# Kernel optimization log

Hardware: AMD Instinct MI355X
Metric: run time of the kernel (lower is better)

Reference implementation:

```python
import jax, jax.numpy as jnp
import numpy as np

NUM_LEVELS = 8
CODEBOOK_SIZE = 1024
D_MODEL = 512


def setup_inputs() -> dict:
    key = jax.random.key(0)
    kx, kc = jax.random.split(key)
    x = jax.random.normal(kx, (8, 4096, D_MODEL), dtype=jnp.float32)
    # stacked embedding tables, one per RVQ level: [L, K, D]
    codebooks = jax.random.normal(kc, (NUM_LEVELS, CODEBOOK_SIZE, D_MODEL), dtype=jnp.float32)
    return {"x": x, "codebooks": codebooks}


def reference(x, codebooks):
    """Residual VQ: per level, nearest-codebook lookup on the residual.

    x: [B, N, D], codebooks: [L, K, D].
    Returns (quantized [B, N, D] with straight-through estimator, indices [B, N, L]).
    """
    residual = x
    q_sum = jnp.zeros_like(x)
    all_indices = []
    for l in range(codebooks.shape[0]):
        cb = codebooks[l]  # [K, D]
        # squared Euclidean distance; argmin matches torch.cdist argmin
        r2 = jnp.sum(residual * residual, axis=-1, keepdims=True)      # [B, N, 1]
        c2 = jnp.sum(cb * cb, axis=-1)                                  # [K]
        cross = jnp.einsum("bnd,kd->bnk", residual, cb)                # [B, N, K]
        dist2 = r2 - 2.0 * cross + c2                                   # [B, N, K]
        idx = jnp.argmin(dist2, axis=-1)                                # [B, N]
        all_indices.append(idx)
        q = cb[idx]                                                     # gather: [B, N, D]
        q_sum = q_sum + q
        residual = residual - q
    # straight-through: forward value is q_sum, gradient flows to x only
    quantized = x + jax.lax.stop_gradient(q_sum - x)
    return quantized, jnp.stack(all_indices, axis=-1)
```

## Files before the change

kernel.cpp:

```cpp
#include <hip/hip_runtime.h>
#include <stdint.h>

#define NLV 8
#define KCB 1024
#define DM  512
#define NTOK (8*4096)
#define BETA 0.00390625f

typedef _Float16 f16;
typedef f16  f16x4 __attribute__((ext_vector_type(4)));
typedef f16  f16x8 __attribute__((ext_vector_type(8)));
typedef float f32x4 __attribute__((ext_vector_type(4)));

typedef __attribute__((address_space(1))) const unsigned int* as1p;
typedef __attribute__((address_space(3))) unsigned int*       as3p;
__device__ __forceinline__ void gll16(const void* g, void* l) {
    __builtin_amdgcn_global_load_lds((as1p)g, (as3p)l, 16, 0, 0);
}

#define VMCNT(n) asm volatile("s_waitcnt vmcnt(" #n ")" ::: "memory")

__global__ void c2_kernel(const float* __restrict__ cbs, float* __restrict__ c2) {
    int row  = blockIdx.x;
    int lane = threadIdx.x;
    const float4* p4 = (const float4*)(cbs + (size_t)row * DM);
    float4 a = p4[lane];
    float4 b = p4[lane + 64];
    float s = a.x*a.x + a.y*a.y + a.z*a.z + a.w*a.w
            + b.x*b.x + b.y*b.y + b.z*b.z + b.w*b.w;
    float t = (float)(f16)a.x + (float)(f16)a.y + (float)(f16)a.z + (float)(f16)a.w
            + (float)(f16)b.x + (float)(f16)b.y + (float)(f16)b.z + (float)(f16)b.w;
    #pragma unroll
    for (int off = 32; off > 0; off >>= 1) {
        s += __shfl_down(s, off, 64);
        t += __shfl_down(t, off, 64);
    }
    if (lane == 0) c2[row] = s + 2.0f * BETA * t;
}

__global__ void split_kernel(const float* __restrict__ src,
                             f16* __restrict__ hi, f16* __restrict__ lo) {
    size_t i = (size_t)blockIdx.x * 256 + threadIdx.x;
    float4 v = ((const float4*)src)[i];
    f16x4 h, l;
    h.x = (f16)v.x; l.x = (f16)((v.x - (float)h.x) + BETA);
    h.y = (f16)v.y; l.y = (f16)((v.y - (float)h.y) + BETA);
    h.z = (f16)v.z; l.z = (f16)((v.z - (float)h.z) + BETA);
    h.w = (f16)v.w; l.w = (f16)((v.w - (float)h.w) + BETA);
    ((f16x4*)hi)[i] = h;
    ((f16x4*)lo)[i] = l;
}

#define MBT  64
#define NCH  256
#define KS   32
#define NTHR 256
#define BUFB 40960

__global__ __launch_bounds__(NTHR, 2)
void rvq_mfma(const float* __restrict__ xin, float* __restrict__ qout,
              const float* __restrict__ cbs,
              const f16* __restrict__ Bhi, const f16* __restrict__ Blo,
              f16* __restrict__ Ahi, f16* __restrict__ Alo,
              const float* __restrict__ c2g, float* __restrict__ idxout,
              int lvl, int is_last)
{
    __shared__ char smem[2 * BUFB];
    const int tid  = threadIdx.x;
    const int lane = tid & 63;
    const int wn   = tid >> 6;
    const int tx   = lane & 15;
    const int q    = lane >> 4;
    const size_t tok0 = (size_t)blockIdx.x * MBT;

    const f16*   Bh_l = Bhi + (size_t)lvl * KCB * DM;
    const f16*   Bl_l = Blo + (size_t)lvl * KCB * DM;
    const float* c2l  = c2g + lvl * KCB;
    const float* cbl  = cbs + (size_t)lvl * KCB * DM;

    const int srow = tid >> 2;
    const int sg   = (tid & 3) ^ ((srow >> 1) & 3);
    const int rsw  = q ^ ((tx >> 1) & 3);

    auto stageA = [&](char* buf, int gk2) {
        const int ko = (gk2 & 15) * KS + sg * 8;
        char* wb = buf + wn * 1024;
        const size_t ga = (tok0 + srow) * (size_t)DM + ko;
        gll16(&Ahi[ga], wb);
        gll16(&Alo[ga], wb + 4096);
    };
    auto stageBh = [&](char* buf, int gk2) {
        const int cb0 = (gk2 >> 4) * NCH;
        const int ko  = (gk2 & 15) * KS + sg * 8;
        char* wb = buf + wn * 1024;
        #pragma unroll
        for (int i = 0; i < 4; ++i)
            gll16(&Bh_l[(size_t)(cb0 + 64 * i + srow) * DM + ko], wb + 8192 + 4096 * i);
    };
    auto stageBl = [&](char* buf, int gk2) {
        const int cb0 = (gk2 >> 4) * NCH;
        const int ko  = (gk2 & 15) * KS + sg * 8;
        char* wb = buf + wn * 1024;
        #pragma unroll
        for (int i = 0; i < 4; ++i)
            gll16(&Bl_l[(size_t)(cb0 + 64 * i + srow) * DM + ko], wb + 24576 + 4096 * i);
    };

    int aoff[4], boff[4];
    #pragma unroll
    for (int i = 0; i < 4; ++i) aoff[i] = (i * 16 + tx) * 64 + rsw * 16;
    #pragma unroll
    for (int j = 0; j < 4; ++j) boff[j] = (wn * 64 + j * 16 + tx) * 64 + rsw * 16;

    float bestv[16];
    int   besti[16];
    #pragma unroll
    for (int t = 0; t < 16; ++t) { bestv[t] = 3.4e38f; besti[t] = 0; }

    stageA(smem, 0); stageBh(smem, 0); stageBl(smem, 0);

    for (int ch = 0; ch < KCB / NCH; ++ch) {
        f32x4 acc[4][4];
        #pragma unroll
        for (int i = 0; i < 4; ++i)
            #pragma unroll
            for (int j = 0; j < 4; ++j) acc[i][j] = (f32x4)0.0f;

        for (int kk = 0; kk < 16; ++kk) {
            const int gk = ch * 16 + kk;
            const int nx = (gk + 1) & 63;
            char* bb = smem + (gk & 1) * BUFB;
            char* bn = smem + ((gk & 1) ^ 1) * BUFB;

            stageA(bn, nx);
            __builtin_amdgcn_sched_barrier(0);
            VMCNT(2);
            __builtin_amdgcn_s_barrier();
            __builtin_amdgcn_sched_barrier(0);

            f16x8 ah[4], al[4], bh[4], bl[4];
            #pragma unroll
            for (int i = 0; i < 4; ++i) ah[i] = *(const f16x8*)(bb + aoff[i]);
            #pragma unroll
            for (int j = 0; j < 4; ++j) bh[j] = *(const f16x8*)(bb + 8192 + boff[j]);

            __builtin_amdgcn_s_setprio(1);
            #pragma unroll
            for (int j = 0; j < 4; ++j)
                #pragma unroll
                for (int i = 0; i < 4; ++i)
                    acc[i][j] = __builtin_amdgcn_mfma_f32_16x16x32_f16(ah[i], bh[j], acc[i][j], 0, 0, 0);
            __builtin_amdgcn_s_setprio(0);

            stageBh(bn, nx);
            __builtin_amdgcn_s_barrier();

            #pragma unroll
            for (int j = 0; j < 4; ++j) bl[j] = *(const f16x8*)(bb + 24576 + boff[j]);

            __builtin_amdgcn_s_setprio(1);
            #pragma unroll
            for (int j = 0; j < 4; ++j)
                #pragma unroll
                for (int i = 0; i < 4; ++i)
                    acc[i][j] = __builtin_amdgcn_mfma_f32_16x16x32_f16(ah[i], bl[j], acc[i][j], 0, 0, 0);
            __builtin_amdgcn_s_setprio(0);

            stageBl(bn, nx);
            __builtin_amdgcn_s_barrier();

            #pragma unroll
            for (int i = 0; i < 4; ++i) al[i] = *(const f16x8*)(bb + 4096 + aoff[i]);

            __builtin_amdgcn_s_setprio(1);
            #pragma unroll
            for (int j = 0; j < 4; ++j)
                #pragma unroll
                for (int i = 0; i < 4; ++i)
                    acc[i][j] = __builtin_amdgcn_mfma_f32_16x16x32_f16(al[i], bh[j], acc[i][j], 0, 0, 0);
            __builtin_amdgcn_s_setprio(0);
        }

        const int cb0 = ch * NCH;
        #pragma unroll
        for (int j = 0; j < 4; ++j) {
            int n = cb0 + wn * 64 + j * 16 + tx;
            float c2v = c2l[n];
            #pragma unroll
            for (int i = 0; i < 4; ++i)
                #pragma unroll
                for (int r = 0; r < 4; ++r) {
                    float s = fmaf(-2.f, acc[i][j][r], c2v);
                    int t = i * 4 + r;
                    if (s < bestv[t]) { bestv[t] = s; besti[t] = n; }
                }
        }
    }

    #pragma unroll
    for (int t = 0; t < 16; ++t) {
        float v = bestv[t]; int bi = besti[t];
        #pragma unroll
        for (int off = 1; off < 16; off <<= 1) {
            float ov = __shfl_xor(v, off, 64);
            int   oi = __shfl_xor(bi, off, 64);
            if (ov < v || (ov == v && oi < bi)) { v = ov; bi = oi; }
        }
        bestv[t] = v; besti[t] = bi;
    }

    float* redV = (float*)smem;
    int*   redI = (int*)(smem + 1024);
    int*   kbst = (int*)(smem + 2048);
    __syncthreads();
    if (tx == 0) {
        #pragma unroll
        for (int i = 0; i < 4; ++i)
            #pragma unroll
            for (int r = 0; r < 4; ++r) {
                int m = i * 16 + q * 4 + r;
                redV[wn * 64 + m] = bestv[i * 4 + r];
                redI[wn * 64 + m] = besti[i * 4 + r];
            }
    }
    __syncthreads();
    if (tid < MBT) {
        float bv = redV[tid]; int bi = redI[tid];
        #pragma unroll
        for (int w = 1; w < 4; ++w) {
            float v  = redV[w * 64 + tid];
            int   ii = redI[w * 64 + tid];
            if (v < bv || (v == bv && ii < bi)) { bv = v; bi = ii; }
        }
        kbst[tid] = bi;
        idxout[(tok0 + tid) * NLV + lvl] = (float)bi;
    }
    __syncthreads();

    #pragma unroll 4
    for (int it = 0; it < 16; ++it) {
        int e  = it * NTHR + tid;
        int t  = e >> 6, d8 = e & 63;
        size_t go = (tok0 + t) * (size_t)DM + d8 * 8;
        f16x8 h8 = *(const f16x8*)&Ahi[go];
        f16x8 l8 = *(const f16x8*)&Alo[go];
        const float* cp = &cbl[(size_t)kbst[t] * DM + d8 * 8];
        float4 c0 = *(const float4*)cp;
        float4 c1 = *(const float4*)(cp + 4);
        float r[8];
        r[0] = (float)h8[0] + ((float)l8[0] - BETA) - c0.x;
        r[1] = (float)h8[1] + ((float)l8[1] - BETA) - c0.y;
        r[2] = (float)h8[2] + ((float)l8[2] - BETA) - c0.z;
        r[3] = (float)h8[3] + ((float)l8[3] - BETA) - c0.w;
        r[4] = (float)h8[4] + ((float)l8[4] - BETA) - c1.x;
        r[5] = (float)h8[5] + ((float)l8[5] - BETA) - c1.y;
        r[6] = (float)h8[6] + ((float)l8[6] - BETA) - c1.z;
        r[7] = (float)h8[7] + ((float)l8[7] - BETA) - c1.w;
        if (is_last) {
            float4 x0 = *(const float4*)&xin[go];
            float4 x1 = *(const float4*)&xin[go + 4];
            float4 q0 = make_float4(x0.x - r[0], x0.y - r[1], x0.z - r[2], x0.w - r[3]);
            float4 q1 = make_float4(x1.x - r[4], x1.y - r[5], x1.z - r[6], x1.w - r[7]);
            *(float4*)&qout[go]     = q0;
            *(float4*)&qout[go + 4] = q1;
        } else {
            f16x8 h, l;
            #pragma unroll
            for (int k = 0; k < 8; ++k) {
                h[k] = (f16)r[k];
                l[k] = (f16)((r[k] - (float)h[k]) + BETA);
            }
            *(f16x8*)&Ahi[go] = h;
            *(f16x8*)&Alo[go] = l;
        }
    }
}

extern "C" void kernel_launch(void* const* d_in, const int* in_sizes, int n_in,
                              void* d_out, int out_size, void* d_ws, size_t ws_size,
                              hipStream_t stream) {
    const float* x   = (const float*)d_in[0];
    const float* cbs = (const float*)d_in[1];
    float* qout   = (float*)d_out;
    float* idxout = qout + (size_t)NTOK * DM;

    const size_t B_ELE = (size_t)NLV * KCB * DM;
    const size_t A_ELE = (size_t)NTOK * DM;

    f16* Bhi = (f16*)d_ws;
    f16* Blo = Bhi + B_ELE;
    f16* Ahi = Blo + B_ELE;
    f16* Alo = Ahi + A_ELE;
    float* c2 = (float*)(Alo + A_ELE);

    split_kernel<<<(int)(B_ELE / 4 / 256), 256, 0, stream>>>(cbs, Bhi, Blo);
    split_kernel<<<(int)(A_ELE / 4 / 256), 256, 0, stream>>>(x, Ahi, Alo);
    c2_kernel<<<NLV * KCB, 64, 0, stream>>>(cbs, c2);

    const int nblocks = NTOK / MBT;
    for (int l = 0; l < NLV; ++l) {
        rvq_mfma<<<nblocks, NTHR, 0, stream>>>(x, qout, cbs,
                                               Bhi, Blo, Ahi, Alo, c2, idxout,
                                               l, (l == NLV - 1) ? 1 : 0);
    }
}
```

Before: 1.147 ms.

## Load codebook B fragments directly into registers, keep only A in LDS

```diff
diff --git a/kernel.cpp b/kernel.cpp
--- a/kernel.cpp
+++ b/kernel.cpp
@@ -55,7 +55,7 @@
 #define NCH  256
 #define KS   32
 #define NTHR 256
-#define BUFB 40960
+#define ABUF 8192
 
 __global__ __launch_bounds__(NTHR, 2)
 void rvq_mfma(const float* __restrict__ xin, float* __restrict__ qout,
@@ -65,7 +65,7 @@
               const float* __restrict__ c2g, float* __restrict__ idxout,
               int lvl, int is_last)
 {
-    __shared__ char smem[2 * BUFB];
+    __shared__ char smem[2 * ABUF];
     const int tid  = threadIdx.x;
     const int lane = tid & 63;
     const int wn   = tid >> 6;
@@ -82,42 +82,45 @@
     const int sg   = (tid & 3) ^ ((srow >> 1) & 3);
     const int rsw  = q ^ ((tx >> 1) & 3);
 
+    const f16* pA0 = Ahi + (tok0 + srow) * (size_t)DM + sg * 8;
+    const f16* pL0 = Alo + (tok0 + srow) * (size_t)DM + sg * 8;
+
     auto stageA = [&](char* buf, int gk2) {
-        const int ko = (gk2 & 15) * KS + sg * 8;
+        const int kOff = (gk2 & 15) * KS;
         char* wb = buf + wn * 1024;
-        const size_t ga = (tok0 + srow) * (size_t)DM + ko;
-        gll16(&Ahi[ga], wb);
-        gll16(&Alo[ga], wb + 4096);
+        gll16(pA0 + kOff, wb);
+        gll16(pL0 + kOff, wb + 4096);
     };
-    auto stageBh = [&](char* buf, int gk2) {
-        const int cb0 = (gk2 >> 4) * NCH;
-        const int ko  = (gk2 & 15) * KS + sg * 8;
-        char* wb = buf + wn * 1024;
-        #pragma unroll
-        for (int i = 0; i < 4; ++i)
-            gll16(&Bh_l[(size_t)(cb0 + 64 * i + srow) * DM + ko], wb + 8192 + 4096 * i);
+
+    int loffB[4];
+    #pragma unroll
+    for (int j = 0; j < 4; ++j)
+        loffB[j] = (wn * 64 + j * 16 + tx) * DM + q * 8;
+
+    auto loadB = [&](int gk2, f16x8 (&bh)[4], f16x8 (&bl)[4]) {
+        const int sOff = ((gk2 >> 4) * NCH) * DM + (gk2 & 15) * KS;
+        const f16* pbh = Bh_l + sOff;
+        const f16* pbl = Bl_l + sOff;
+        #pragma unroll
+        for (int j = 0; j < 4; ++j) {
+            bh[j] = *(const f16x8*)(pbh + loffB[j]);
+            bl[j] = *(const f16x8*)(pbl + loffB[j]);
+        }
     };
-    auto stageBl = [&](char* buf, int gk2) {
-        const int cb0 = (gk2 >> 4) * NCH;
-        const int ko  = (gk2 & 15) * KS + sg * 8;
-        char* wb = buf + wn * 1024;
-        #pragma unroll
-        for (int i = 0; i < 4; ++i)
-            gll16(&Bl_l[(size_t)(cb0 + 64 * i + srow) * DM + ko], wb + 24576 + 4096 * i);
-    };
-
-    int aoff[4], boff[4];
+
+    int aoff[4];
     #pragma unroll
     for (int i = 0; i < 4; ++i) aoff[i] = (i * 16 + tx) * 64 + rsw * 16;
-    #pragma unroll
-    for (int j = 0; j < 4; ++j) boff[j] = (wn * 64 + j * 16 + tx) * 64 + rsw * 16;
 
     float bestv[16];
     int   besti[16];
     #pragma unroll
     for (int t = 0; t < 16; ++t) { bestv[t] = 3.4e38f; besti[t] = 0; }
 
-    stageA(smem, 0); stageBh(smem, 0); stageBl(smem, 0);
+    f16x8 bhE[4], blE[4], bhO[4], blO[4];
+
+    loadB(0, bhE, blE);
+    stageA(smem, 0);
 
     for (int ch = 0; ch < KCB / NCH; ++ch) {
         f32x4 acc[4][4];
@@ -126,59 +129,48 @@
             #pragma unroll
             for (int j = 0; j < 4; ++j) acc[i][j] = (f32x4)0.0f;
 
-        for (int kk = 0; kk < 16; ++kk) {
-            const int gk = ch * 16 + kk;
+        auto kbody = [&](int gk, f16x8 (&bhc)[4], f16x8 (&blc)[4],
+                         f16x8 (&bhn)[4], f16x8 (&bln)[4]) {
             const int nx = (gk + 1) & 63;
-            char* bb = smem + (gk & 1) * BUFB;
-            char* bn = smem + ((gk & 1) ^ 1) * BUFB;
-
+            char* bb = smem + (gk & 1) * ABUF;
+            char* bn = smem + ((gk & 1) ^ 1) * ABUF;
+
+            loadB(nx, bhn, bln);
             stageA(bn, nx);
             __builtin_amdgcn_sched_barrier(0);
-            VMCNT(2);
+            VMCNT(10);
             __builtin_amdgcn_s_barrier();
             __builtin_amdgcn_sched_barrier(0);
 
-            f16x8 ah[4], al[4], bh[4], bl[4];
+            f16x8 ah[4], al[4];
             #pragma unroll
             for (int i = 0; i < 4; ++i) ah[i] = *(const f16x8*)(bb + aoff[i]);
             #pragma unroll
-            for (int j = 0; j < 4; ++j) bh[j] = *(const f16x8*)(bb + 8192 + boff[j]);
+            for (int i = 0; i < 4; ++i) al[i] = *(const f16x8*)(bb + 4096 + aoff[i]);
 
             __builtin_amdgcn_s_setprio(1);
             #pragma unroll
             for (int j = 0; j < 4; ++j)
                 #pragma unroll
                 for (int i = 0; i < 4; ++i)
-                    acc[i][j] = __builtin_amdgcn_mfma_f32_16x16x32_f16(ah[i], bh[j], acc[i][j], 0, 0, 0);
+                    acc[i][j] = __builtin_amdgcn_mfma_f32_16x16x32_f16(ah[i], bhc[j], acc[i][j], 0, 0, 0);
+            #pragma unroll
+            for (int j = 0; j < 4; ++j)
+                #pragma unroll
+                for (int i = 0; i < 4; ++i)
+                    acc[i][j] = __builtin_amdgcn_mfma_f32_16x16x32_f16(ah[i], blc[j], acc[i][j], 0, 0, 0);
+            #pragma unroll
+            for (int j = 0; j < 4; ++j)
+                #pragma unroll
+                for (int i = 0; i < 4; ++i)
+                    acc[i][j] = __builtin_amdgcn_mfma_f32_16x16x32_f16(al[i], bhc[j], acc[i][j], 0, 0, 0);
             __builtin_amdgcn_s_setprio(0);
-
-            stageBh(bn, nx);
-            __builtin_amdgcn_s_barrier();
-
-            #pragma unroll
-            for (int j = 0; j < 4; ++j) bl[j] = *(const f16x8*)(bb + 24576 + boff[j]);
-
-            __builtin_amdgcn_s_setprio(1);
-            #pragma unroll
-            for (int j = 0; j < 4; ++j)
-                #pragma unroll
-                for (int i = 0; i < 4; ++i)
-                    acc[i][j] = __builtin_amdgcn_mfma_f32_16x16x32_f16(ah[i], bl[j], acc[i][j], 0, 0, 0);
-            __builtin_amdgcn_s_setprio(0);
-
-            stageBl(bn, nx);
-            __builtin_amdgcn_s_barrier();
-
-            #pragma unroll
-            for (int i = 0; i < 4; ++i) al[i] = *(const f16x8*)(bb + 4096 + aoff[i]);
-
-            __builtin_amdgcn_s_setprio(1);
-            #pragma unroll
-            for (int j = 0; j < 4; ++j)
-                #pragma unroll
-                for (int i = 0; i < 4; ++i)
-                    acc[i][j] = __builtin_amdgcn_mfma_f32_16x16x32_f16(al[i], bh[j], acc[i][j], 0, 0, 0);
-            __builtin_amdgcn_s_setprio(0);
+        };
+
+        for (int kp = 0; kp < 8; ++kp) {
+            const int gk = ch * 16 + kp * 2;
+            kbody(gk,     bhE, blE, bhO, blO);
+            kbody(gk + 1, bhO, blO, bhE, blE);
         }
 
         const int cb0 = ch * NCH;
```

Result: slower. 1.360 ms (+18.6%).
